# Kernel tuning notes

Hardware: AMD Instinct MI355X
Metric: run time of the kernel (lower is better)

The kernel has to match this reference:

```python
import jax, jax.numpy as jnp
import numpy as np

NUM_HEADS = 16
LORA_SCALE = 32.0 / 8.0  # alpha / rank
ROPE_BASE = 10000.0


def make_sincos(seq_len, dim):
    # theta[t, j] = t / base**( (2j)/dim ), shapes (T, dim//2)
    pos = jnp.arange(seq_len, dtype=jnp.float32)
    i = jnp.arange(0, dim, 2, dtype=jnp.float32) / dim
    theta = pos[:, None] / (ROPE_BASE ** i[None, :])
    return jnp.sin(theta), jnp.cos(theta)


def apply_rope(x, sin, cos):
    # x: (B, h, T, d) with interleaved even/odd rotation pairs
    x_even = x[..., 0::2]
    x_odd = x[..., 1::2]
    rot_even = x_even * cos - x_odd * sin
    rot_odd = x_even * sin + x_odd * cos
    return jnp.stack([rot_even, rot_odd], axis=-1).reshape(x.shape)


def setup_inputs() -> dict:
    key = jax.random.key(0)
    ks = jax.random.split(key, 9)
    B, T, D, R = 4, 2048, 1024, 8
    s = 1.0 / np.sqrt(D)
    return {
        "query": jax.random.normal(ks[0], (B, T, D), dtype=jnp.float32),
        "wq": jax.random.normal(ks[1], (D, D), dtype=jnp.float32) * s,
        "wk": jax.random.normal(ks[2], (D, D), dtype=jnp.float32) * s,
        "wv": jax.random.normal(ks[3], (D, D), dtype=jnp.float32) * s,
        "wo": jax.random.normal(ks[4], (D, D), dtype=jnp.float32) * s,
        "Aq": jax.random.normal(ks[5], (D, R), dtype=jnp.float32) * s,
        "Bq": jax.random.normal(ks[6], (R, D), dtype=jnp.float32) * 0.01,
        "Av": jax.random.normal(ks[7], (D, R), dtype=jnp.float32) * s,
        "Bv": jax.random.normal(ks[8], (R, D), dtype=jnp.float32) * 0.01,
    }


def reference(query, wq, wk, wv, wo, Aq, Bq, Av, Bv):
    B, T, D = query.shape
    H = NUM_HEADS
    dh = D // H

    # fused base + LoRA projections (self-attention: key=value=query)
    q = query @ wq + ((query @ Aq) @ Bq) * LORA_SCALE
    k = query @ wk
    v = query @ wv + ((query @ Av) @ Bv) * LORA_SCALE

    def split(x):  # (B,T,D) -> (B,H,T,dh)
        return x.reshape(B, T, H, dh).transpose(0, 2, 1, 3)

    q, k, v = split(q), split(k), split(v)

    sin, cos = make_sincos(T, dh)
    q = apply_rope(q, sin, cos)
    k = apply_rope(k, sin, cos)

    scores = jnp.einsum("bhqd,bhkd->bhqk", q, k) / jnp.sqrt(jnp.float32(dh))
    causal = jnp.triu(jnp.ones((T, T), dtype=bool), k=1)  # mask == 1 -> blocked
    scores = jnp.where(causal[None, None], jnp.float32(-1e9), scores)
    attn = jax.nn.softmax(scores, axis=-1)  # dropout p=0 -> identity

    out = jnp.einsum("bhqk,bhkd->bhqd", attn, v)
    out = out.transpose(0, 2, 1, 3).reshape(B, T, D)
    return out @ wo
```

## Files before the change

### kernel.cpp

```cpp
#include <hip/hip_runtime.h>
#include <cstdint>

#define B_  4
#define T_  2048
#define D_  1024
#define H_  16
#define DH_ 64
#define R_  8
#define M_  (B_*T_)
#define LORA_SCALE 4.0f

typedef __attribute__((ext_vector_type(8))) short    bf16x8;
typedef __attribute__((ext_vector_type(4))) short    bf16x4;
typedef __attribute__((ext_vector_type(4))) float    f32x4;
typedef __attribute__((ext_vector_type(4))) uint32_t u32x4;

__device__ inline uint16_t f2b(float f) {
    uint32_t x = __float_as_uint(f);
    return (uint16_t)((x + 0x7fffu + ((x >> 16) & 1u)) >> 16);
}
__device__ inline float b2f(uint16_t u) { return __uint_as_float(((uint32_t)u) << 16); }

__device__ __forceinline__ uint32_t cvtpk(float lo, float hi) {
    uint32_t r;
    asm("v_cvt_pk_bf16_f32 %0, %1, %2" : "=v"(r) : "v"(lo), "v"(hi));
    return r;
}
__device__ __forceinline__ float max3f(float a, float b, float c) {
    float r;
    asm("v_max3_f32 %0, %1, %2, %3" : "=v"(r) : "v"(a), "v"(b), "v"(c));
    return r;
}

__device__ __forceinline__ void gld_lds16(const uint16_t* g, uint16_t* l) {
    __builtin_amdgcn_global_load_lds(
        (const __attribute__((address_space(1))) void*)g,
        (__attribute__((address_space(3))) void*)l, 16, 0, 0);
}

__global__ void cast_x_kernel(const float* __restrict__ x, uint16_t* __restrict__ out) {
    int g = blockIdx.x * 256 + threadIdx.x;
    const float4* xv = (const float4*)x;
    float4 a = xv[2 * g], b = xv[2 * g + 1];
    union { u32x4 v; uint16_t s[8]; } u;
    u.s[0] = f2b(a.x); u.s[1] = f2b(a.y); u.s[2] = f2b(a.z); u.s[3] = f2b(a.w);
    u.s[4] = f2b(b.x); u.s[5] = f2b(b.y); u.s[6] = f2b(b.z); u.s[7] = f2b(b.w);
    ((u32x4*)out)[g] = u.v;
}

__global__ void make_wt_kernel(const float* __restrict__ wq, const float* __restrict__ wk,
                               const float* __restrict__ wv, const float* __restrict__ wo,
                               const float* __restrict__ Aq, const float* __restrict__ Bq,
                               const float* __restrict__ Av, const float* __restrict__ Bv,
                               uint16_t* __restrict__ Wt) {
    __shared__ float tile[64][65];
    int mat = blockIdx.z;
    int n0 = blockIdx.x * 64, k0 = blockIdx.y * 64;
    const float* W  = (mat == 0) ? wq : (mat == 1) ? wk : (mat == 2) ? wv : wo;
    const float* Ap = (mat == 0) ? Aq : (mat == 2) ? Av : nullptr;
    const float* Bp = (mat == 0) ? Bq : (mat == 2) ? Bv : nullptr;
    int t = threadIdx.x;
    int r = t >> 2, c0 = (t & 3) * 16;
    int k = k0 + r;
    #pragma unroll
    for (int j = 0; j < 16; j++) {
        int n = n0 + c0 + j;
        float v = W[(size_t)k * D_ + n];
        if (Ap) {
            float acc = 0.f;
            #pragma unroll
            for (int rr = 0; rr < R_; rr++) acc += Ap[k * R_ + rr] * Bp[rr * D_ + n];
            v += LORA_SCALE * acc;
        }
        tile[r][c0 + j] = v;
    }
    __syncthreads();
    int nl = t >> 2, ks = (t & 3) * 16;
    union { uint16_t s[16]; u32x4 v[2]; } uo;
    #pragma unroll
    for (int j = 0; j < 16; j++) uo.s[j] = f2b(tile[ks + j][nl]);
    uint16_t* dst = Wt + (size_t)mat * D_ * D_ + (size_t)(n0 + nl) * D_ + k0 + ks;
    *(u32x4*)&dst[0] = uo.v[0];
    *(u32x4*)&dst[8] = uo.v[1];
}

template <bool OUT_F32>
__global__ __launch_bounds__(256)
void gemm_bt_kernel(const uint16_t* __restrict__ A, const uint16_t* __restrict__ Bt,
                    uint16_t* __restrict__ Cb, float* __restrict__ Cf,
                    int Mdim, int Ndim, int Kdim) {
    __shared__ uint16_t At[128 * 32];
    __shared__ uint16_t Bs[128 * 32];
    int tid = threadIdx.x;
    int wave = tid >> 6, lane = tid & 63, quad = lane >> 4, l15 = lane & 15;
    int rowBase = blockIdx.y * 128, colBase = blockIdx.x * 128;
    int wRow = (wave >> 1) * 64, wCol = (wave & 1) * 64;
    int srow0 = tid >> 2, sseg0 = (tid & 3) * 8;
    int srow1 = (tid + 256) >> 2;
    f32x4 acc[4][4] = {};
    for (int kb = 0; kb < Kdim; kb += 32) {
        gld_lds16(&A [(size_t)(rowBase + srow0) * Kdim + kb + sseg0], &At[srow0 * 32 + sseg0]);
        gld_lds16(&A [(size_t)(rowBase + srow1) * Kdim + kb + sseg0], &At[srow1 * 32 + sseg0]);
        gld_lds16(&Bt[(size_t)(colBase + srow0) * Kdim + kb + sseg0], &Bs[srow0 * 32 + sseg0]);
        gld_lds16(&Bt[(size_t)(colBase + srow1) * Kdim + kb + sseg0], &Bs[srow1 * 32 + sseg0]);
        __syncthreads();
        bf16x8 af[4], bfr[4];
        #pragma unroll
        for (int m = 0; m < 4; m++) af[m]  = *(const bf16x8*)&At[(wRow + m * 16 + l15) * 32 + quad * 8];
        #pragma unroll
        for (int n = 0; n < 4; n++) bfr[n] = *(const bf16x8*)&Bs[(wCol + n * 16 + l15) * 32 + quad * 8];
        #pragma unroll
        for (int m = 0; m < 4; m++)
            #pragma unroll
            for (int n = 0; n < 4; n++)
                acc[m][n] = __builtin_amdgcn_mfma_f32_16x16x32_bf16(af[m], bfr[n], acc[m][n], 0, 0, 0);
        __syncthreads();
    }
    #pragma unroll
    for (int m = 0; m < 4; m++) {
        int row = rowBase + wRow + m * 16 + quad * 4;
        #pragma unroll
        for (int n = 0; n < 4; n++) {
            int col = colBase + wCol + n * 16 + l15;
            #pragma unroll
            for (int r = 0; r < 4; r++) {
                float v = acc[m][n][r];
                if (OUT_F32) Cf[(size_t)(row + r) * Ndim + col] = v;
                else         Cb[(size_t)(row + r) * Ndim + col] = f2b(v);
            }
        }
    }
}

__global__ void rope_kernel(const uint16_t* __restrict__ qkv,
                            uint16_t* __restrict__ Qr, uint16_t* __restrict__ Kr) {
    int g = blockIdx.x * 256 + threadIdx.x;
    int i  = g & 31;
    int t  = (g >> 5) & (T_ - 1);
    int bh = g >> 16;
    int h = bh & 15, b = bh >> 4;
    size_t rowoff = ((size_t)(b * T_ + t)) * 3072 + h * 64 + 2 * i;
    uint32_t qp = *(const uint32_t*)&qkv[rowoff];
    uint32_t kp = *(const uint32_t*)&qkv[rowoff + 1024];
    float qe = b2f((uint16_t)qp), qo = b2f((uint16_t)(qp >> 16));
    float ke = b2f((uint16_t)kp), ko = b2f((uint16_t)(kp >> 16));
    float inv = exp2f(-(float)i * (13.2877123795494f / 32.f));
    float th = (float)t * inv;
    float s = sinf(th), c = cosf(th);
    const float SC = 0.125f * 1.44269504089f;
    uint32_t qw = (uint32_t)f2b((qe * c - qo * s) * SC)
                | ((uint32_t)f2b((qe * s + qo * c) * SC) << 16);
    uint32_t kw = (uint32_t)f2b(ke * c - ko * s) | ((uint32_t)f2b(ke * s + ko * c) << 16);
    size_t o = ((size_t)bh * T_ + t) * 64 + 2 * i;
    *(uint32_t*)&Qr[o] = qw;
    int d = 2 * i;
    size_t kidx = ((size_t)bh * T_ + t) * 64 + ((((d >> 3) ^ (t & 7)) << 3) | (d & 7));
    *(uint32_t*)&Kr[kidx] = kw;
}

__global__ void vtrans_kernel(const uint16_t* __restrict__ qkv, uint16_t* __restrict__ Vt) {
    __shared__ uint16_t tile[32][72];
    int bh = blockIdx.y, t0 = blockIdx.x * 32;
    int b = bh >> 4, h = bh & 15;
    int tid = threadIdx.x;
    int r = tid >> 3, c8 = (tid & 7) * 8;
    *(u32x4*)&tile[r][c8] =
        *(const u32x4*)&qkv[((size_t)(b * T_ + t0 + r)) * 3072 + 2048 + h * 64 + c8];
    __syncthreads();
    int d = tid >> 2, t8 = (tid & 3) * 8;
    union { uint16_t s[8]; u32x4 v; } uu;
    #pragma unroll
    for (int j = 0; j < 8; j++) uu.s[j] = tile[t8 + j][d];
    int tt = t0 + t8;
    int c  = (tt & 63) >> 3;
    int phys = (c ^ (d & 7)) & 7;
    size_t vidx = (size_t)bh * 64 * T_ + (size_t)(tt >> 6) * 4096 + d * 64 + phys * 8;
    *(u32x4*)&Vt[vidx] = uu.v;
}

#define PSTR 72

__device__ __forceinline__ f32x4 mfma16(bf16x8 a, bf16x8 b, f32x4 c) {
    return __builtin_amdgcn_mfma_f32_16x16x32_bf16(a, b, c, 0, 0, 0);
}

template <bool MASKED>
__device__ __forceinline__ void attn_chunk_sw(
    const uint16_t* __restrict__ Kst, const uint16_t* __restrict__ Vst,
    uint16_t* __restrict__ Pw, int nact, int base_kmq,
    bf16x8 aQ0, bf16x8 aQ1, int l15, int quad,
    f32x4 (&Oacc)[4], float& mrow, float& lrow)
{
    int lx = l15 & 7;
    f32x4 sacc[4];
    if (MASKED) {
        #pragma unroll
        for (int n = 0; n < 4; n++) sacc[n] = f32x4{0.f, 0.f, 0.f, 0.f};
    }
    #pragma unroll
    for (int n = 0; n < 4; n++) {
        if (MASKED && n >= nact) continue;
        int rowK = (n * 16 + l15) * 64;
        bf16x8 kv0 = *(const bf16x8*)&Kst[rowK + ((quad ^ lx) << 3)];
        bf16x8 kv1 = *(const bf16x8*)&Kst[rowK + (((quad + 4) ^ lx) << 3)];
        f32x4 s = {};
        s = mfma16(kv0, aQ0, s);
        s = mfma16(kv1, aQ1, s);
        sacc[n] = s;
    }
    float mx = -1e30f;
    #pragma unroll
    for (int n = 0; n < 4; n++) {
        if (MASKED && n >= nact) continue;
        if (MASKED) {
            #pragma unroll
            for (int r = 0; r < 4; r++) {
                int kmq = base_kmq + n * 16 + quad * 4 + r;
                if (kmq > 0) sacc[n][r] = -1e30f;
            }
        }
        float t = max3f(sacc[n][0], sacc[n][1], sacc[n][2]);
        mx = max3f(mx, t, sacc[n][3]);
    }
    mx = fmaxf(mx, __shfl_xor(mx, 16, 64));
    mx = fmaxf(mx, __shfl_xor(mx, 32, 64));
    if (!__all(mx <= mrow + 8.f)) {
        float mnew = fmaxf(mrow, mx);
        float alpha = exp2f(mrow - mnew);
        #pragma unroll
        for (int m = 0; m < 4; m++)
            #pragma unroll
            for (int r = 0; r < 4; r++) Oacc[m][r] *= alpha;
        lrow *= alpha;
        mrow = mnew;
    }
    float sum = 0.f;
    #pragma unroll
    for (int n = 0; n < 4; n++) {
        if (MASKED && n >= nact) continue;
        #pragma unroll
        for (int r = 0; r < 4; r++) {
            float e = exp2f(sacc[n][r] - mrow);
            sacc[n][r] = e;
            sum += e;
        }
    }
    sum += __shfl_xor(sum, 16, 64);
    sum += __shfl_xor(sum, 32, 64);
    lrow += sum;
    #pragma unroll
    for (int n = 0; n < 4; n++) {
        if (MASKED && n >= nact) continue;
        uint2 pk;
        pk.x = cvtpk(sacc[n][0], sacc[n][1]);
        pk.y = cvtpk(sacc[n][2], sacc[n][3]);
        *(uint2*)&Pw[l15 * PSTR + n * 16 + quad * 4] = pk;
    }
    if (MASKED && (nact & 1)) {
        uint2 z; z.x = 0u; z.y = 0u;
        *(uint2*)&Pw[l15 * PSTR + nact * 16 + quad * 4] = z;
    }
    int ssact = MASKED ? ((nact + 1) >> 1) : 2;
    #pragma unroll
    for (int ss = 0; ss < 2; ss++) {
        if (MASKED && ss >= ssact) continue;
        bf16x8 bP = *(const bf16x8*)&Pw[l15 * PSTR + ss * 32 + quad * 8];
        int cl = ss * 4 + quad;
        int phys = (cl ^ lx) & 7;
        #pragma unroll
        for (int m = 0; m < 4; m++) {
            bf16x8 aV = *(const bf16x8*)&Vst[(m * 16 + l15) * 64 + (phys << 3)];
            Oacc[m] = mfma16(aV, bP, Oacc[m]);
        }
    }
}

__global__ __launch_bounds__(256, 6)
void attn_kernel(const uint16_t* __restrict__ Qr, const uint16_t* __restrict__ Kr,
                 const uint16_t* __restrict__ Vt, uint16_t* __restrict__ Obuf) {
    __shared__ uint16_t KLDS[64 * 64];
    __shared__ uint16_t VLDS[64 * 64];
    __shared__ uint16_t Pl[4][16 * PSTR];
    int id  = blockIdx.x;
    int xcd = id & 7, grp = id >> 3;
    int bh  = xcd * 8 + (grp & 7);
    int qt  = 31 - (grp >> 3);
    int b = bh >> 4, h = bh & 15;
    int tid = threadIdx.x, wave = tid >> 6, lane = tid & 63, quad = lane >> 4, l15 = lane & 15;
    const uint16_t* Qbase = Qr + (size_t)bh * T_ * 64;
    const uint16_t* Kbase = Kr + (size_t)bh * T_ * 64;
    const uint16_t* Vbase = Vt + (size_t)bh * 64 * T_;
    uint16_t* Pw = &Pl[wave][0];
    int q0w = qt * 64 + wave * 16;
    bf16x8 aQ0 = *(const bf16x8*)&Qbase[(size_t)(q0w + l15) * 64 + quad * 8];
    bf16x8 aQ1 = *(const bf16x8*)&Qbase[(size_t)(q0w + l15) * 64 + 32 + quad * 8];
    f32x4 Oacc[4] = {};
    float mrow = -1e30f, lrow = 0.f;
    int nch = qt + 1;
    int klim = q0w + 15;
    int idx0 = tid, idx1 = tid + 256;
    for (int c = 0; c < nch; c++) {
        int k0 = c * 64;
        __syncthreads();
        const uint16_t* gK = Kbase + (size_t)k0 * 64;
        const uint16_t* gV = Vbase + (size_t)(k0 >> 6) * 4096;
        gld_lds16(gK + idx0 * 8, &KLDS[idx0 * 8]);
        gld_lds16(gK + idx1 * 8, &KLDS[idx1 * 8]);
        gld_lds16(gV + idx0 * 8, &VLDS[idx0 * 8]);
        gld_lds16(gV + idx1 * 8, &VLDS[idx1 * 8]);
        __syncthreads();
        if (c == nch - 1) {
            int nact = ((klim - k0) >> 4) + 1;
            attn_chunk_sw<true>(KLDS, VLDS, Pw, nact, k0 - q0w - l15,
                                aQ0, aQ1, l15, quad, Oacc, mrow, lrow);
        } else {
            attn_chunk_sw<false>(KLDS, VLDS, Pw, 4, 0,
                                 aQ0, aQ1, l15, quad, Oacc, mrow, lrow);
        }
    }
    float invl = 1.0f / lrow;
    size_t obase = ((size_t)(b * T_ + q0w + l15)) * D_ + h * 64;
    #pragma unroll
    for (int m = 0; m < 4; m++) {
        uint2 ob;
        ob.x = cvtpk(Oacc[m][0] * invl, Oacc[m][1] * invl);
        ob.y = cvtpk(Oacc[m][2] * invl, Oacc[m][3] * invl);
        *(uint2*)&Obuf[obase + m * 16 + quad * 4] = ob;
    }
}

extern "C" void kernel_launch(void* const* d_in, const int* in_sizes, int n_in,
                              void* d_out, int out_size, void* d_ws, size_t ws_size,
                              hipStream_t stream) {
    const float* query = (const float*)d_in[0];
    const float* wq = (const float*)d_in[1];
    const float* wk = (const float*)d_in[2];
    const float* wv = (const float*)d_in[3];
    const float* wo = (const float*)d_in[4];
    const float* Aq = (const float*)d_in[5];
    const float* Bq = (const float*)d_in[6];
    const float* Av = (const float*)d_in[7];
    const float* Bv = (const float*)d_in[8];
    float* out = (float*)d_out;

    const size_t MB = 1ull << 20;
    if (ws_size < 120 * MB) return;
    char* ws = (char*)d_ws;
    uint16_t* Xbf = (uint16_t*)(ws);
    uint16_t* Wt  = (uint16_t*)(ws + 16 * MB);
    uint16_t* qkv = (uint16_t*)(ws + 24 * MB);
    uint16_t* Qr  = (uint16_t*)(ws + 72 * MB);
    uint16_t* Kr  = (uint16_t*)(ws + 88 * MB);
    uint16_t* Vt  = (uint16_t*)(ws + 104 * MB);
    uint16_t* Obuf = qkv;

    cast_x_kernel<<<4096, 256, 0, stream>>>(query, Xbf);
    make_wt_kernel<<<dim3(16, 16, 4), 256, 0, stream>>>(wq, wk, wv, wo, Aq, Bq, Av, Bv, Wt);
    gemm_bt_kernel<false><<<dim3(3072 / 128, M_ / 128), 256, 0, stream>>>(
        Xbf, Wt, qkv, nullptr, M_, 3072, D_);
    rope_kernel<<<16384, 256, 0, stream>>>(qkv, Qr, Kr);
    vtrans_kernel<<<dim3(T_ / 32, B_ * H_), 256, 0, stream>>>(qkv, Vt);
    attn_kernel<<<2048, 256, 0, stream>>>(Qr, Kr, Vt, Obuf);
    gemm_bt_kernel<true><<<dim3(D_ / 128, M_ / 128), 256, 0, stream>>>(
        Obuf, Wt + 3ull * D_ * D_, nullptr, out, M_, D_, D_);
}
```

Baseline: 310.5 us.

## Process two 16-row query groups per wave in attention to reuse K/V fragments

The attention block drops from four waves with 16 query rows each to two waves with 32 query rows each. Each wave now runs two independent online-softmax groups that share every K and V fragment read from LDS, which halves LDS traffic per MFMA. The cost is roughly double the accumulator and score registers per wave, and fewer waves per block for hiding latency. Launch bounds move to 128 threads with a lower occupancy target.

```diff
diff --git a/kernel.cpp b/kernel.cpp
--- a/kernel.cpp
+++ b/kernel.cpp
@@ -185,102 +185,120 @@
 }
 
 template <bool MASKED>
-__device__ __forceinline__ void attn_chunk_sw(
+__device__ __forceinline__ void attn_chunk2(
     const uint16_t* __restrict__ Kst, const uint16_t* __restrict__ Vst,
-    uint16_t* __restrict__ Pw, int nact, int base_kmq,
-    bf16x8 aQ0, bf16x8 aQ1, int l15, int quad,
-    f32x4 (&Oacc)[4], float& mrow, float& lrow)
+    uint16_t* __restrict__ Pw, int nact0, int bkmq0,
+    const bf16x8 (&aQ)[2][2], int l15, int quad,
+    f32x4 (&Oacc)[2][4], float (&mrow)[2], float (&lrow)[2])
 {
     int lx = l15 & 7;
-    f32x4 sacc[4];
+    int nact1 = MASKED ? nact0 + 1 : 4;
+    f32x4 sacc[2][4];
     if (MASKED) {
         #pragma unroll
-        for (int n = 0; n < 4; n++) sacc[n] = f32x4{0.f, 0.f, 0.f, 0.f};
+        for (int g = 0; g < 2; g++)
+            #pragma unroll
+            for (int n = 0; n < 4; n++) sacc[g][n] = f32x4{0.f, 0.f, 0.f, 0.f};
     }
     #pragma unroll
     for (int n = 0; n < 4; n++) {
-        if (MASKED && n >= nact) continue;
+        if (MASKED && n >= nact1) continue;
         int rowK = (n * 16 + l15) * 64;
         bf16x8 kv0 = *(const bf16x8*)&Kst[rowK + ((quad ^ lx) << 3)];
         bf16x8 kv1 = *(const bf16x8*)&Kst[rowK + (((quad + 4) ^ lx) << 3)];
-        f32x4 s = {};
-        s = mfma16(kv0, aQ0, s);
-        s = mfma16(kv1, aQ1, s);
-        sacc[n] = s;
-    }
-    float mx = -1e30f;
-    #pragma unroll
-    for (int n = 0; n < 4; n++) {
-        if (MASKED && n >= nact) continue;
-        if (MASKED) {
+        if (!MASKED || n < nact0) {
+            f32x4 s = {};
+            s = mfma16(kv0, aQ[0][0], s);
+            s = mfma16(kv1, aQ[0][1], s);
+            sacc[0][n] = s;
+        }
+        {
+            f32x4 s = {};
+            s = mfma16(kv0, aQ[1][0], s);
+            s = mfma16(kv1, aQ[1][1], s);
+            sacc[1][n] = s;
+        }
+    }
+    #pragma unroll
+    for (int g = 0; g < 2; g++) {
+        int nag = MASKED ? (g ? nact1 : nact0) : 4;
+        int bkm = bkmq0 - g * 16;
+        float mx = -1e30f;
+        #pragma unroll
+        for (int n = 0; n < 4; n++) {
+            if (MASKED && n >= nag) continue;
+            if (MASKED) {
+                #pragma unroll
+                for (int r = 0; r < 4; r++) {
+                    int kmq = bkm + n * 16 + quad * 4 + r;
+                    if (kmq > 0) sacc[g][n][r] = -1e30f;
+                }
+            }
+            float t = max3f(sacc[g][n][0], sacc[g][n][1], sacc[g][n][2]);
+            mx = max3f(mx, t, sacc[g][n][3]);
+        }
+        mx = fmaxf(mx, __shfl_xor(mx, 16, 64));
+        mx = fmaxf(mx, __shfl_xor(mx, 32, 64));
+        if (!__all(mx <= mrow[g] + 8.f)) {
+            float mnew = fmaxf(mrow[g], mx);
+            float alpha = exp2f(mrow[g] - mnew);
+            #pragma unroll
+            for (int m = 0; m < 4; m++)
+                #pragma unroll
+                for (int r = 0; r < 4; r++) Oacc[g][m][r] *= alpha;
+            lrow[g] *= alpha;
+            mrow[g] = mnew;
+        }
+        float sum = 0.f;
+        #pragma unroll
+        for (int n = 0; n < 4; n++) {
+            if (MASKED && n >= nag) continue;
             #pragma unroll
             for (int r = 0; r < 4; r++) {
-                int kmq = base_kmq + n * 16 + quad * 4 + r;
-                if (kmq > 0) sacc[n][r] = -1e30f;
+                float e = exp2f(sacc[g][n][r] - mrow[g]);
+                sacc[g][n][r] = e;
+                sum += e;
             }
         }
-        float t = max3f(sacc[n][0], sacc[n][1], sacc[n][2]);
-        mx = max3f(mx, t, sacc[n][3]);
-    }
-    mx = fmaxf(mx, __shfl_xor(mx, 16, 64));
-    mx = fmaxf(mx, __shfl_xor(mx, 32, 64));
-    if (!__all(mx <= mrow + 8.f)) {
-        float mnew = fmaxf(mrow, mx);
-        float alpha = exp2f(mrow - mnew);
-        #pragma unroll
-        for (int m = 0; m < 4; m++)
-            #pragma unroll
-            for (int r = 0; r < 4; r++) Oacc[m][r] *= alpha;
-        lrow *= alpha;
-        mrow = mnew;
-    }
-    float sum = 0.f;
-    #pragma unroll
-    for (int n = 0; n < 4; n++) {
-        if (MASKED && n >= nact) continue;
-        #pragma unroll
-        for (int r = 0; r < 4; r++) {
-            float e = exp2f(sacc[n][r] - mrow);
-            sacc[n][r] = e;
-            sum += e;
-        }
-    }
-    sum += __shfl_xor(sum, 16, 64);
-    sum += __shfl_xor(sum, 32, 64);
-    lrow += sum;
-    #pragma unroll
-    for (int n = 0; n < 4; n++) {
-        if (MASKED && n >= nact) continue;
-        uint2 pk;
-        pk.x = cvtpk(sacc[n][0], sacc[n][1]);
-        pk.y = cvtpk(sacc[n][2], sacc[n][3]);
-        *(uint2*)&Pw[l15 * PSTR + n * 16 + quad * 4] = pk;
-    }
-    if (MASKED && (nact & 1)) {
-        uint2 z; z.x = 0u; z.y = 0u;
-        *(uint2*)&Pw[l15 * PSTR + nact * 16 + quad * 4] = z;
-    }
-    int ssact = MASKED ? ((nact + 1) >> 1) : 2;
+        sum += __shfl_xor(sum, 16, 64);
+        sum += __shfl_xor(sum, 32, 64);
+        lrow[g] += sum;
+        #pragma unroll
+        for (int n = 0; n < 4; n++) {
+            if (MASKED && n >= nag) continue;
+            uint2 pk;
+            pk.x = cvtpk(sacc[g][n][0], sacc[g][n][1]);
+            pk.y = cvtpk(sacc[g][n][2], sacc[g][n][3]);
+            *(uint2*)&Pw[(g * 16 + l15) * PSTR + n * 16 + quad * 4] = pk;
+        }
+        if (MASKED && (nag & 1)) {
+            uint2 z; z.x = 0u; z.y = 0u;
+            *(uint2*)&Pw[(g * 16 + l15) * PSTR + nag * 16 + quad * 4] = z;
+        }
+    }
+    int ssact = MASKED ? ((nact1 + 1) >> 1) : 2;
     #pragma unroll
     for (int ss = 0; ss < 2; ss++) {
         if (MASKED && ss >= ssact) continue;
-        bf16x8 bP = *(const bf16x8*)&Pw[l15 * PSTR + ss * 32 + quad * 8];
+        bf16x8 bP0 = *(const bf16x8*)&Pw[l15 * PSTR + ss * 32 + quad * 8];
+        bf16x8 bP1 = *(const bf16x8*)&Pw[(16 + l15) * PSTR + ss * 32 + quad * 8];
         int cl = ss * 4 + quad;
         int phys = (cl ^ lx) & 7;
         #pragma unroll
         for (int m = 0; m < 4; m++) {
             bf16x8 aV = *(const bf16x8*)&Vst[(m * 16 + l15) * 64 + (phys << 3)];
-            Oacc[m] = mfma16(aV, bP, Oacc[m]);
-        }
-    }
-}
-
-__global__ __launch_bounds__(256, 6)
+            Oacc[0][m] = mfma16(aV, bP0, Oacc[0][m]);
+            Oacc[1][m] = mfma16(aV, bP1, Oacc[1][m]);
+        }
+    }
+}
+
+__global__ __launch_bounds__(128, 3)
 void attn_kernel(const uint16_t* __restrict__ Qr, const uint16_t* __restrict__ Kr,
                  const uint16_t* __restrict__ Vt, uint16_t* __restrict__ Obuf) {
     __shared__ uint16_t KLDS[64 * 64];
     __shared__ uint16_t VLDS[64 * 64];
-    __shared__ uint16_t Pl[4][16 * PSTR];
+    __shared__ uint16_t Pl[2][32 * PSTR];
     int id  = blockIdx.x;
     int xcd = id & 7, grp = id >> 3;
     int bh  = xcd * 8 + (grp & 7);
@@ -291,41 +309,47 @@
     const uint16_t* Kbase = Kr + (size_t)bh * T_ * 64;
     const uint16_t* Vbase = Vt + (size_t)bh * 64 * T_;
     uint16_t* Pw = &Pl[wave][0];
-    int q0w = qt * 64 + wave * 16;
-    bf16x8 aQ0 = *(const bf16x8*)&Qbase[(size_t)(q0w + l15) * 64 + quad * 8];
-    bf16x8 aQ1 = *(const bf16x8*)&Qbase[(size_t)(q0w + l15) * 64 + 32 + quad * 8];
-    f32x4 Oacc[4] = {};
-    float mrow = -1e30f, lrow = 0.f;
+    int q0w = qt * 64 + wave * 32;
+    bf16x8 aQ[2][2];
+    #pragma unroll
+    for (int g = 0; g < 2; g++) {
+        aQ[g][0] = *(const bf16x8*)&Qbase[(size_t)(q0w + g * 16 + l15) * 64 + quad * 8];
+        aQ[g][1] = *(const bf16x8*)&Qbase[(size_t)(q0w + g * 16 + l15) * 64 + 32 + quad * 8];
+    }
+    f32x4 Oacc[2][4] = {};
+    float mrow[2] = {-1e30f, -1e30f}, lrow[2] = {0.f, 0.f};
     int nch = qt + 1;
-    int klim = q0w + 15;
-    int idx0 = tid, idx1 = tid + 256;
     for (int c = 0; c < nch; c++) {
         int k0 = c * 64;
         __syncthreads();
         const uint16_t* gK = Kbase + (size_t)k0 * 64;
         const uint16_t* gV = Vbase + (size_t)(k0 >> 6) * 4096;
-        gld_lds16(gK + idx0 * 8, &KLDS[idx0 * 8]);
-        gld_lds16(gK + idx1 * 8, &KLDS[idx1 * 8]);
-        gld_lds16(gV + idx0 * 8, &VLDS[idx0 * 8]);
-        gld_lds16(gV + idx1 * 8, &VLDS[idx1 * 8]);
+        #pragma unroll
+        for (int j = 0; j < 4; j++) {
+            gld_lds16(gK + (tid + j * 128) * 8, &KLDS[(tid + j * 128) * 8]);
+            gld_lds16(gV + (tid + j * 128) * 8, &VLDS[(tid + j * 128) * 8]);
+        }
         __syncthreads();
         if (c == nch - 1) {
-            int nact = ((klim - k0) >> 4) + 1;
-            attn_chunk_sw<true>(KLDS, VLDS, Pw, nact, k0 - q0w - l15,
-                                aQ0, aQ1, l15, quad, Oacc, mrow, lrow);
+            int nact0 = ((q0w + 15 - k0) >> 4) + 1;
+            attn_chunk2<true>(KLDS, VLDS, Pw, nact0, k0 - q0w - l15,
+                              aQ, l15, quad, Oacc, mrow, lrow);
         } else {
-            attn_chunk_sw<false>(KLDS, VLDS, Pw, 4, 0,
-                                 aQ0, aQ1, l15, quad, Oacc, mrow, lrow);
-        }
-    }
-    float invl = 1.0f / lrow;
-    size_t obase = ((size_t)(b * T_ + q0w + l15)) * D_ + h * 64;
-    #pragma unroll
-    for (int m = 0; m < 4; m++) {
-        uint2 ob;
-        ob.x = cvtpk(Oacc[m][0] * invl, Oacc[m][1] * invl);
-        ob.y = cvtpk(Oacc[m][2] * invl, Oacc[m][3] * invl);
-        *(uint2*)&Obuf[obase + m * 16 + quad * 4] = ob;
+            attn_chunk2<false>(KLDS, VLDS, Pw, 0, 0,
+                               aQ, l15, quad, Oacc, mrow, lrow);
+        }
+    }
+    #pragma unroll
+    for (int g = 0; g < 2; g++) {
+        float invl = 1.0f / lrow[g];
+        size_t obase = ((size_t)(b * T_ + q0w + g * 16 + l15)) * D_ + h * 64;
+        #pragma unroll
+        for (int m = 0; m < 4; m++) {
+            uint2 ob;
+            ob.x = cvtpk(Oacc[g][m][0] * invl, Oacc[g][m][1] * invl);
+            ob.y = cvtpk(Oacc[g][m][2] * invl, Oacc[g][m][3] * invl);
+            *(uint2*)&Obuf[obase + m * 16 + quad * 4] = ob;
+        }
     }
 }
 
@@ -360,7 +384,7 @@
         Xbf, Wt, qkv, nullptr, M_, 3072, D_);
     rope_kernel<<<16384, 256, 0, stream>>>(qkv, Qr, Kr);
     vtrans_kernel<<<dim3(T_ / 32, B_ * H_), 256, 0, stream>>>(qkv, Vt);
-    attn_kernel<<<2048, 256, 0, stream>>>(Qr, Kr, Vt, Obuf);
+    attn_kernel<<<2048, 128, 0, stream>>>(Qr, Kr, Vt, Obuf);
     gemm_bt_kernel<true><<<dim3(D_ / 128, M_ / 128), 256, 0, stream>>>(
         Obuf, Wt + 3ull * D_ * D_, nullptr, out, M_, D_, D_);
 }
```

Measured after the change: 316.8 us. +2.0%, slower.
